# Optimization experiments

Hardware: AMD Instinct MI355X
Metric: run time of the kernel (lower is better)

## Reference

```python
import jax, jax.numpy as jnp
import numpy as np
from jax import lax

B, V, C, H, W = 2, 8, 64, 128, 128
A = 256
C3 = 3 * C + 2  # 194 input channels for refine/confidence branches
CO = 3 * C      # 192 output channels of branch_refine
GROUPS = 8      # _group_count(192, 8) == 8
HID = max(4, CO // 4)  # 48 hidden channels in ChannelGate2d


def _conv3(x, w, b):
    y = lax.conv_general_dilated(x, w, (1, 1), 'SAME',
                                 dimension_numbers=('NCHW', 'OIHW', 'NCHW'))
    return y + b[None, :, None, None]


def _group_norm(x, scale, bias, groups, eps=1e-5):
    b, c, h, w = x.shape
    xg = x.reshape(b, groups, c // groups, h, w)
    mu = xg.mean(axis=(2, 3, 4), keepdims=True)
    var = xg.var(axis=(2, 3, 4), keepdims=True)
    xn = ((xg - mu) / jnp.sqrt(var + eps)).reshape(b, c, h, w)
    return xn * scale[None, :, None, None] + bias[None, :, None, None]


def _channel_gate(x, w1, b1, w2, b2):
    pooled = x.mean(axis=(2, 3))                     # [B,C]
    h = jax.nn.silu(pooled @ w1.T + b1)              # [B,HID]
    gate = jax.nn.sigmoid(h @ w2.T + b2)             # [B,C]
    return x * (0.5 + gate)[:, :, None, None]


def _conv_block(x, p):
    h = jax.nn.silu(_group_norm(_conv3(x, p['c1w'], p['c1b']), p['g1s'], p['g1b'], GROUPS))
    h = jax.nn.silu(_group_norm(_conv3(h, p['c2w'], p['c2b']), p['g2s'], p['g2b'], GROUPS))
    h = _channel_gate(h, p['gw1'], p['gb1'], p['gw2'], p['gb2'])
    res = jnp.einsum('bchw,oc->bohw', x, p['rpw']) + p['rpb'][None, :, None, None]
    return h + jnp.tanh(p['rs']) * res


def _fuse(vf, uvs, masks, importance, atlas_size):
    # vf:[B,V,C,H,W] uvs:[B,V,H,W,2] masks:[B,V,1,H,W] importance:[B,V]
    b, v, c, h, w = vf.shape
    P = atlas_size * atlas_size
    weights = jnp.maximum(importance.astype(vf.dtype), 0.0)
    finite = jnp.isfinite(uvs).all(axis=-1)                 # [B,V,H,W]
    valid = (masks[:, :, 0] > 0.5) & finite & (weights[:, :, None, None] > 0.0)
    safe = jnp.where(finite[..., None], uvs, 0.0)
    xi = jnp.round(jnp.clip(safe[..., 0], 0.0, 1.0) * (atlas_size - 1)).astype(jnp.int32)
    yi = jnp.round((1.0 - jnp.clip(safe[..., 1], 0.0, 1.0)) * (atlas_size - 1)).astype(jnp.int32)
    idx = (yi * atlas_size + xi).reshape(b, v * h * w)      # [B,N]
    wvalid = valid.astype(vf.dtype) * weights[:, :, None, None]
    feat = (vf * wvalid[:, :, None]).transpose(0, 2, 1, 3, 4).reshape(b, c, v * h * w)
    cnt = wvalid.reshape(b, v * h * w)

    def per_sample(f, cc, i):
        atlas = jax.ops.segment_sum(f.T, i, num_segments=P).T   # [C,P]
        counts = jax.ops.segment_sum(cc, i, num_segments=P)     # [P]
        return atlas, counts

    atlas, counts = jax.vmap(per_sample)(feat, cnt, idx)
    atlas = atlas.reshape(b, c, atlas_size, atlas_size)
    counts = counts.reshape(b, 1, atlas_size, atlas_size)
    fused = atlas / jnp.maximum(counts, 1.0)
    return fused, (counts > 0).astype(vf.dtype)


def _normalize_per_sample(t, eps=1e-6):
    scale = jnp.maximum(t.reshape(t.shape[0], -1).max(axis=1), eps)
    return jnp.clip(t / scale[:, None, None, None], 0.0, 1.0)


def setup_inputs() -> dict:
    key = jax.random.key(0)
    ks = jax.random.split(key, 20)
    inp = {
        'encoded_views': jax.random.normal(ks[0], (B, V, C, H, W), jnp.float32),
        'view_uvs': jax.random.uniform(ks[1], (B, V, H, W, 2), jnp.float32),
        'view_masks': jax.random.uniform(ks[2], (B, V, 1, H, W), jnp.float32),
        'w_global': jax.random.uniform(ks[3], (B, V), jnp.float32),
        'w_boundary': jax.random.uniform(ks[4], (B, V), jnp.float32),
        'w_highlight': jax.random.uniform(ks[5], (B, V), jnp.float32),
        'atlas_size': A,
        # ConvBlock params (random instead of zero-init so all paths are exercised)
        'c1w': jax.random.normal(ks[6], (CO, C3, 3, 3), jnp.float32) * 0.02,
        'c1b': jnp.zeros((CO,), jnp.float32),
        'g1s': jnp.ones((CO,), jnp.float32),
        'g1b': jnp.zeros((CO,), jnp.float32),
        'c2w': jax.random.normal(ks[7], (CO, CO, 3, 3), jnp.float32) * 0.02,
        'c2b': jnp.zeros((CO,), jnp.float32),
        'g2s': jnp.ones((CO,), jnp.float32),
        'g2b': jnp.zeros((CO,), jnp.float32),
        'gw1': jax.random.normal(ks[8], (HID, CO), jnp.float32) * 0.05,
        'gb1': jnp.zeros((HID,), jnp.float32),
        'gw2': jax.random.normal(ks[9], (CO, HID), jnp.float32) * 0.05,
        'gb2': jnp.zeros((CO,), jnp.float32),
        'rpw': jax.random.normal(ks[10], (CO, C3), jnp.float32) * 0.05,
        'rpb': jnp.zeros((CO,), jnp.float32),
        'rs': jnp.array(0.3, jnp.float32),
        'conf_w': jax.random.normal(ks[11], (3, C3), jnp.float32) * 0.05,
        'conf_b': jnp.zeros((3,), jnp.float32),
        'mix_scale': jnp.array(0.5, jnp.float32),
    }
    return inp


def reference(encoded_views, view_uvs, view_masks, w_global, w_boundary, w_highlight,
              atlas_size, c1w, c1b, g1s, g1b, c2w, c2b, g2s, g2b,
              gw1, gb1, gw2, gb2, rpw, rpb, rs, conf_w, conf_b, mix_scale):
    p = dict(c1w=c1w, c1b=c1b, g1s=g1s, g1b=g1b, c2w=c2w, c2b=c2b, g2s=g2s, g2b=g2b,
             gw1=gw1, gb1=gb1, gw2=gw2, gb2=gb2, rpw=rpw, rpb=rpb, rs=rs)
    g_feat, g_val = _fuse(encoded_views, view_uvs, view_masks, w_global, atlas_size)
    b_feat, b_val = _fuse(encoded_views, view_uvs, view_masks, w_boundary, atlas_size)
    h_feat, h_val = _fuse(encoded_views, view_uvs, view_masks, w_highlight, atlas_size)
    coverage = jnp.clip((g_val + b_val + h_val) / 3.0, 0.0, 1.0)
    stack = jnp.stack([g_feat, b_feat, h_feat], axis=1)     # [B,3,C,A,A]
    uncertainty = jnp.sqrt(stack.var(axis=1).mean(axis=1, keepdims=True))
    uncertainty = _normalize_per_sample(uncertainty) * coverage
    ctx = jnp.concatenate([g_feat, b_feat, h_feat, coverage, uncertainty], axis=1)
    refine = _conv_block(ctx, p)
    rg, rb, rh = jnp.split(refine, 3, axis=1)
    conf = jax.nn.sigmoid(jnp.einsum('bchw,oc->bohw', ctx, conf_w) + conf_b[None, :, None, None])
    ms = jnp.tanh(mix_scale)
    g_out = g_feat + ms * rg * conf[:, 0:1]
    b_out = b_feat + ms * rb * conf[:, 1:2]
    h_out = h_feat + ms * rh * conf[:, 2:3]
    return (g_out, b_out, h_out, coverage, uncertainty, conf)
```

## Files before the change

kernel.cpp:

```cpp
#include <hip/hip_runtime.h>
#include <math.h>

#define B_ 2
#define V_ 8
#define C_ 64
#define HW_ 16384
#define A_ 256
#define P_ 65536
#define CO_ 192
#define CPG_ 24
#define NG_ 8
#define ICP1 224
#define ICP2 192

#define OFF_ACC   0ull
#define SZ_ACC    (2ull*65536*192*4)
#define OFF_CNT   (OFF_ACC + SZ_ACC)
#define SZ_CNT    (2ull*3*65536*4)
#define OFF_CTXB  (OFF_CNT + SZ_CNT)
#define SZ_CTXB   (2ull*65536*224*2)
#define OFF_H1A   (OFF_CTXB + SZ_CTXB)
#define SZ_H1A    (2ull*65536*192*2)
#define OFF_W1    (OFF_H1A + SZ_H1A)
#define SZ_W1     (9ull*192*224*2)
#define OFF_W2    (OFF_W1 + SZ_W1)
#define SZ_W2     (9ull*192*192*2)
#define OFF_SM    (OFF_W2 + SZ_W2 + 256)

#define SM_STATS1 0
#define SM_STATS2 256
#define SM_SCALE  512
#define SM_POOLED 1024
#define SM_GATE   2560
#define SM_RAWU   8192

#define OUT_B    8388608
#define OUT_COV  25165824
#define OUT_UNC  25296896
#define OUT_CONF 25427968

typedef __attribute__((ext_vector_type(4))) float f32x4;
typedef __attribute__((ext_vector_type(8))) short bf16x8;

__device__ __forceinline__ float sigmoidf_(float x){ return 1.f/(1.f+expf(-x)); }
__device__ __forceinline__ float bf2f(unsigned short h){ return __uint_as_float(((unsigned)h)<<16); }
__device__ __forceinline__ unsigned short f2bf(float f){
  unsigned u = __float_as_uint(f);
  return (unsigned short)((u + 0x7fffu + ((u>>16)&1u)) >> 16);
}

__global__ __launch_bounds__(256) void k_prep(const float* __restrict__ c1w,
    const float* __restrict__ c2w, unsigned short* __restrict__ w1p, unsigned short* __restrict__ w2p)
{
  int idx = blockIdx.x*256 + threadIdx.x;
  const int N1 = 9*192*224;
  if (idx < N1){
    int ic = idx % 224; int oc = (idx/224) % 192; int k = idx/(224*192);
    float v = (ic < 194) ? c1w[(size_t)(oc*194+ic)*9 + k] : 0.f;
    w1p[idx] = f2bf(v);
  } else {
    int i2 = idx - N1;
    if (i2 < 9*192*192){
      int ic = i2 % 192; int oc = (i2/192) % 192; int k = i2/(192*192);
      w2p[i2] = f2bf(c2w[(size_t)(oc*192+ic)*9 + k]);
    }
  }
}

__global__ __launch_bounds__(256) void k_fuse(const float* __restrict__ vf,
    const float* __restrict__ uvs, const float* __restrict__ masks,
    const float* __restrict__ wgp, const float* __restrict__ wbp, const float* __restrict__ whp,
    float* __restrict__ acc, float* __restrict__ cnt)
{
  __shared__ __align__(16) float sf[64*65];
  __shared__ int sidx[64];
  __shared__ int svalid[64];
  __shared__ float sw[3];
  int t = threadIdx.x;
  int pix0 = blockIdx.x*64;
  int b   = pix0 / (V_*HW_);
  int rem = pix0 % (V_*HW_);
  int v   = rem / HW_;
  int p2  = rem % HW_;
  size_t vbase = ((size_t)(b*V_+v))*C_*HW_;
  for (int i=0;i<16;i++){
    int f = t + i*256;
    int c = f>>6, px = f&63;
    sf[c*65+px] = vf[vbase + (size_t)c*HW_ + p2 + px];
  }
  if (t<64){
    const float* u2 = uvs + (((size_t)(b*V_+v))*HW_ + p2 + t)*2;
    float ux = u2[0], uy = u2[1];
    int fin = isfinite(ux) && isfinite(uy);
    float su = fin?ux:0.f, svv = fin?uy:0.f;
    float cu = fminf(fmaxf(su,0.f),1.f);
    float cv = fminf(fmaxf(svv,0.f),1.f);
    int xi = (int)rintf(cu*255.f);
    int yi = (int)rintf((1.f-cv)*255.f);
    sidx[t] = yi*256+xi;
    float m = masks[((size_t)(b*V_+v))*HW_ + p2 + t];
    svalid[t] = (m>0.5f) && fin;
  }
  if (t<3){
    const float* wp = (t==0)?wgp:((t==1)?wbp:whp);
    sw[t] = fmaxf(wp[b*V_+v], 0.f);
  }
  __syncthreads();
  int wave = t>>6, lane = t&63;
  float w0 = sw[0], w1 = sw[1], w2 = sw[2];
  for (int i=0;i<16;i++){
    int px = wave*16+i;
    if (!svalid[px]) continue;
    int bin = sidx[px];
    float val = sf[lane*65+px];
    size_t base = ((size_t)b*P_ + bin)*192;
    if (w0>0.f) atomicAdd(&acc[base + lane],        val*w0);
    if (w1>0.f) atomicAdd(&acc[base + 64 + lane],   val*w1);
    if (w2>0.f) atomicAdd(&acc[base + 128 + lane],  val*w2);
    if (lane<3){
      float wv = sw[lane];
      if (wv>0.f) atomicAdd(&cnt[((size_t)(b*3+lane))*P_ + bin], wv);
    }
  }
}

__global__ __launch_bounds__(256) void k_finalize(const float* __restrict__ acc,
      const float* __restrict__ cnt, unsigned short* __restrict__ ctxb,
      float* __restrict__ out_cov, float* __restrict__ raw_unc, int* __restrict__ scale)
{
  __shared__ __align__(16) float sv[64*193];
  __shared__ float sc[3][64];
  __shared__ float up[256];
  __shared__ float s_cov[64];
  __shared__ float s_unc[64];
  int t = threadIdx.x;
  int bin0 = blockIdx.x*64;
  int b = bin0 >> 16;
  int p0 = bin0 & 65535;
  size_t abase = ((size_t)b*P_ + p0)*192;
  for (int i=0;i<48;i++){
    int f = t + i*256;
    int bl = f/192, c = f - bl*192;
    sv[bl*193+c] = acc[abase + f];
  }
  if (t<192){
    int br = t>>6, bl = t&63;
    sc[br][bl] = cnt[((size_t)(b*3+br))*P_ + p0 + bl];
  }
  __syncthreads();
  {
    int bl = t>>2, q = t&3;
    float dg = 1.f/fmaxf(sc[0][bl],1.f);
    float db = 1.f/fmaxf(sc[1][bl],1.f);
    float dh = 1.f/fmaxf(sc[2][bl],1.f);
    float s = 0.f;
    for (int j=0;j<16;j++){
      int c = q*16+j;
      float fg = sv[bl*193+c]*dg;
      float fb = sv[bl*193+64+c]*db;
      float fh = sv[bl*193+128+c]*dh;
      sv[bl*193+c]=fg; sv[bl*193+64+c]=fb; sv[bl*193+128+c]=fh;
      float m = (fg+fb+fh)*(1.f/3.f);
      float d0=fg-m, d1=fb-m, d2=fh-m;
      s += d0*d0+d1*d1+d2*d2;
    }
    up[t] = s;
  }
  __syncthreads();
  if (t<64){
    float tot = up[t*4]+up[t*4+1]+up[t*4+2]+up[t*4+3];
    float u = sqrtf(tot*(1.f/192.f));
    float vg = sc[0][t]>0.f?1.f:0.f;
    float vb = sc[1][t]>0.f?1.f:0.f;
    float vh = sc[2][t]>0.f?1.f:0.f;
    float cov = fminf(fmaxf((vg+vb+vh)*(1.f/3.f),0.f),1.f);
    s_cov[t] = cov; s_unc[t] = u;
    out_cov[(size_t)b*P_ + p0 + t] = cov;
    raw_unc[(size_t)b*P_ + p0 + t] = u;
    atomicMax(&scale[b], __float_as_int(u));
  }
  __syncthreads();
  for (int f=t; f<1792; f+=256){
    int cg = f % 28, bl = f / 28;
    int c0 = cg*8;
    unsigned short h[8];
    #pragma unroll
    for (int j=0;j<8;j++){
      int c = c0+j;
      float vv;
      if (c < 192)      vv = sv[bl*193+c];
      else if (c==192)  vv = s_cov[bl];
      else if (c==193)  vv = s_unc[bl];
      else              vv = 0.f;
      h[j] = f2bf(vv);
    }
    *(uint4*)&ctxb[((size_t)b*P_ + p0 + bl)*ICP1 + c0] = *(uint4*)h;
  }
}

__global__ __launch_bounds__(256) void k_norm_unc(unsigned short* __restrict__ ctxb,
    const int* __restrict__ scale, const float* __restrict__ raw_unc,
    const float* __restrict__ out_cov, float* __restrict__ out_unc)
{
  int tid = blockIdx.x*256 + threadIdx.x;
  int b = tid >> 16;
  float s = fmaxf(__int_as_float(scale[b]), 1e-6f);
  float u = raw_unc[tid];
  float cov = out_cov[tid];
  float un = fminf(fmaxf(u/s,0.f),1.f)*cov;
  out_unc[tid] = un;
  ctxb[(size_t)tid*ICP1 + 193] = f2bf(un);
}

template<int ICP, int CHUNKS>
__global__ __launch_bounds__(256,4) void k_conv3(const unsigned short* __restrict__ X,
    const unsigned short* __restrict__ Wp, const float* __restrict__ bias, float* __restrict__ Y)
{
  __shared__ short s_in[258*32];
  __shared__ short s_w[192*32];
  int t = threadIdx.x;
  int y0 = blockIdx.x;
  int oc0 = blockIdx.y*64;
  int b = blockIdx.z;
  int wv = t>>6, lane = t&63, l15 = lane&15, quad = lane>>4;
  f32x4 acc[4][4];
  #pragma unroll
  for (int mt=0;mt<4;mt++){
    float4 bv = *(const float4*)&bias[oc0 + mt*16 + quad*4];
    f32x4 iv; iv.x=bv.x; iv.y=bv.y; iv.z=bv.z; iv.w=bv.w;
    #pragma unroll
    for (int nt=0;nt<4;nt++) acc[mt][nt]=iv;
  }
  const unsigned short* Xb = X + (size_t)b*P_*ICP;
  for (int ch=0; ch<CHUNKS; ++ch){
    int ic0 = ch*32;
    for (int ky=0; ky<3; ky++){
      int gy = y0 + ky - 1;
      if ((unsigned)gy >= 256u) continue;
      __syncthreads();
      for (int f=t; f<1032; f+=256){
        int icq = f&3, xi = f>>2;
        int gx = xi - 1;
        uint4 vval = make_uint4(0,0,0,0);
        if ((unsigned)gx < 256u)
          vval = *(const uint4*)&Xb[(size_t)(gy*256+gx)*ICP + ic0 + icq*8];
        *(uint4*)&s_in[xi*32 + ((icq ^ ((xi>>1)&3)))*8] = vval;
      }
      for (int f=t; f<768; f+=256){
        int icq = f&3, oc = (f>>2)&63, kx = f>>8;
        uint4 vval = *(const uint4*)&Wp[(size_t)((ky*3+kx)*192 + oc0 + oc)*ICP + ic0 + icq*8];
        int r = kx*64 + oc;
        *(uint4*)&s_w[r*32 + ((icq ^ ((r>>1)&3)))*8] = vval;
      }
      __syncthreads();
      #pragma unroll
      for (int kx=0;kx<3;kx++){
        bf16x8 Af[4], Bf[4];
        #pragma unroll
        for (int mt=0;mt<4;mt++){
          int r = kx*64 + mt*16 + l15;
          Af[mt] = *(const bf16x8*)&s_w[r*32 + (((quad ^ ((r>>1)&3)))&3)*8];
        }
        #pragma unroll
        for (int nt=0;nt<4;nt++){
          int r = wv*64 + nt*16 + l15 + kx;
          Bf[nt] = *(const bf16x8*)&s_in[r*32 + (((quad ^ ((r>>1)&3)))&3)*8];
        }
        #pragma unroll
        for (int mt=0;mt<4;mt++)
          #pragma unroll
          for (int nt=0;nt<4;nt++)
            acc[mt][nt] = __builtin_amdgcn_mfma_f32_16x16x32_bf16(Af[mt], Bf[nt], acc[mt][nt], 0, 0, 0);
      }
    }
  }
  float* Yb = Y + (size_t)b*P_*192;
  #pragma unroll
  for (int mt=0;mt<4;mt++){
    int oc = oc0 + mt*16 + quad*4;
    #pragma unroll
    for (int nt=0;nt<4;nt++){
      int px = wv*64 + nt*16 + l15;
      *(f32x4*)&Yb[(size_t)(y0*256+px)*192 + oc] = acc[mt][nt];
    }
  }
}

__global__ __launch_bounds__(256) void k_gn_stats(const float* __restrict__ x, double* __restrict__ stats)
{
  int b = blockIdx.y; int y0 = blockIdx.x*2;
  const float* base = x + ((size_t)b*P_ + y0*256)*192;
  int t = threadIdx.x;
  double s1[3]={0,0,0}, s2[3]={0,0,0};
  for (int j=0;j<96;j++){
    int f4 = t + j*256;
    float4 v = *(const float4*)&base[(size_t)f4*4];
    int r = j - (j/3)*3;
    s1[r] += (double)v.x + (double)v.y + (double)v.z + (double)v.w;
    s2[r] += (double)v.x*v.x + (double)v.y*v.y + (double)v.z*v.z + (double)v.w*v.w;
  }
  __shared__ double red[16];
  if (t<16) red[t]=0.0;
  __syncthreads();
  #pragma unroll
  for (int r=0;r<3;r++){
    int c = (4*t + 64*r) % 192;
    int g = c/24;
    atomicAdd(&red[g*2],   s1[r]);
    atomicAdd(&red[g*2+1], s2[r]);
  }
  __syncthreads();
  if (t<8){
    atomicAdd(&stats[(b*8+t)*2],   red[t*2]);
    atomicAdd(&stats[(b*8+t)*2+1], red[t*2+1]);
  }
}

__global__ __launch_bounds__(256) void k_gn1_apply(const float* __restrict__ x, const double* __restrict__ stats,
    const float* __restrict__ gs, const float* __restrict__ gb, unsigned short* __restrict__ y)
{
  size_t i8 = ((size_t)blockIdx.x*256 + threadIdx.x)*8;
  int b = (int)(i8 / ((size_t)192*P_));
  int c = (int)(i8 % 192);
  int bg = b*8 + c/24;
  const double N = 24.0*65536.0;
  double mu = stats[bg*2]/N;
  double var = stats[bg*2+1]/N - mu*mu;
  float rstd = 1.0f/sqrtf((float)var + 1e-5f);
  float mean = (float)mu;
  float4 sA = *(const float4*)&gs[c];
  float4 sB = *(const float4*)&gs[c+4];
  float4 bA = *(const float4*)&gb[c];
  float4 bB = *(const float4*)&gb[c+4];
  float4 v0 = *(const float4*)&x[i8];
  float4 v1 = *(const float4*)&x[i8+4];
  float xin[8] = {v0.x,v0.y,v0.z,v0.w,v1.x,v1.y,v1.z,v1.w};
  float scl[8] = {sA.x,sA.y,sA.z,sA.w,sB.x,sB.y,sB.z,sB.w};
  float bia[8] = {bA.x,bA.y,bA.z,bA.w,bB.x,bB.y,bB.z,bB.w};
  unsigned short h[8];
  #pragma unroll
  for (int i=0;i<8;i++){
    float xn = (xin[i]-mean)*rstd*scl[i] + bia[i];
    h[i] = f2bf(xn*sigmoidf_(xn));
  }
  *(uint4*)&y[i8] = *(uint4*)h;
}

__global__ __launch_bounds__(256) void k_gn2_apply(float* __restrict__ x, const double* __restrict__ stats,
    const float* __restrict__ gs, const float* __restrict__ gb)
{
  size_t i8 = ((size_t)blockIdx.x*256 + threadIdx.x)*8;
  int b = (int)(i8 / ((size_t)192*P_));
  int c = (int)(i8 % 192);
  int bg = b*8 + c/24;
  const double N = 24.0*65536.0;
  double mu = stats[bg*2]/N;
  double var = stats[bg*2+1]/N - mu*mu;
  float rstd = 1.0f/sqrtf((float)var + 1e-5f);
  float mean = (float)mu;
  float4 sA = *(const float4*)&gs[c];
  float4 sB = *(const float4*)&gs[c+4];
  float4 bA = *(const float4*)&gb[c];
  float4 bB = *(const float4*)&gb[c+4];
  float4 v0 = *(const float4*)&x[i8];
  float4 v1 = *(const float4*)&x[i8+4];
  float xin[8] = {v0.x,v0.y,v0.z,v0.w,v1.x,v1.y,v1.z,v1.w};
  float scl[8] = {sA.x,sA.y,sA.z,sA.w,sB.x,sB.y,sB.z,sB.w};
  float bia[8] = {bA.x,bA.y,bA.z,bA.w,bB.x,bB.y,bB.z,bB.w};
  #pragma unroll
  for (int i=0;i<8;i++){
    float xn = (xin[i]-mean)*rstd*scl[i] + bia[i];
    xin[i] = xn*sigmoidf_(xn);
  }
  *(float4*)&x[i8]   = make_float4(xin[0],xin[1],xin[2],xin[3]);
  *(float4*)&x[i8+4] = make_float4(xin[4],xin[5],xin[6],xin[7]);
}

__global__ __launch_bounds__(256) void k_pool(const float* __restrict__ x, float* __restrict__ pooled)
{
  int b = blockIdx.y; int y0 = blockIdx.x*4;
  const float* base = x + ((size_t)b*P_ + y0*256)*192;
  int t = threadIdx.x;
  float4 p[3];
  #pragma unroll
  for (int r=0;r<3;r++) p[r] = make_float4(0.f,0.f,0.f,0.f);
  for (int j=0;j<192;j++){
    int f4 = t + j*256;
    float4 v = *(const float4*)&base[(size_t)f4*4];
    int r = j - (j/3)*3;
    p[r].x += v.x; p[r].y += v.y; p[r].z += v.z; p[r].w += v.w;
  }
  __shared__ float pl[192];
  if (t<192) pl[t]=0.f;
  __syncthreads();
  #pragma unroll
  for (int r=0;r<3;r++){
    int c = (4*t + 64*r) % 192;
    atomicAdd(&pl[c],   p[r].x);
    atomicAdd(&pl[c+1], p[r].y);
    atomicAdd(&pl[c+2], p[r].z);
    atomicAdd(&pl[c+3], p[r].w);
  }
  __syncthreads();
  if (t<192) atomicAdd(&pooled[b*192+t], pl[t]*(1.f/65536.f));
}

__global__ void k_gate(const float* __restrict__ pooled, const float* __restrict__ gw1,
    const float* __restrict__ gb1, const float* __restrict__ gw2, const float* __restrict__ gb2,
    float* __restrict__ gatef)
{
  __shared__ float hb[2*48];
  int t = threadIdx.x;
  if (t<96){
    int b=t/48, j=t%48;
    float a = gb1[j];
    for (int c=0;c<192;c++) a = fmaf(pooled[b*192+c], gw1[j*192+c], a);
    hb[t] = a*sigmoidf_(a);
  }
  __syncthreads();
  for (int i=t;i<384;i+=256){
    int b=i/192, c=i%192;
    float a = gb2[c];
    for (int j=0;j<48;j++) a = fmaf(hb[b*48+j], gw2[c*48+j], a);
    gatef[i] = 0.5f + sigmoidf_(a);
  }
}

__global__ __launch_bounds__(256) void k_conf(const unsigned short* __restrict__ ctxb,
    const float* __restrict__ cw, const float* __restrict__ cbias, float* __restrict__ out_conf)
{
  __shared__ float scw[3*224];
  int t = threadIdx.x;
  for (int f=t; f<672; f+=256){
    int c = f % 224, o = f / 224;
    scw[f] = (c<194) ? cw[o*194 + c] : 0.f;
  }
  __syncthreads();
  int tid = blockIdx.x*256 + t;
  int b = tid >> 16, p = tid & 65535;
  const unsigned short* cp = ctxb + ((size_t)b*P_ + p)*ICP1;
  float a0 = cbias[0], a1 = cbias[1], a2 = cbias[2];
  for (int q=0;q<28;q++){
    uint4 v = *(const uint4*)&cp[q*8];
    unsigned wd[4] = {v.x,v.y,v.z,v.w};
    #pragma unroll
    for (int j=0;j<8;j++){
      unsigned bits = wd[j>>1];
      float xf = (j&1) ? __uint_as_float(bits & 0xffff0000u) : __uint_as_float(bits<<16);
      int c = q*8+j;
      a0 = fmaf(xf, scw[c],       a0);
      a1 = fmaf(xf, scw[224+c],   a1);
      a2 = fmaf(xf, scw[448+c],   a2);
    }
  }
  out_conf[((size_t)(b*3+0))*P_ + p] = sigmoidf_(a0);
  out_conf[((size_t)(b*3+1))*P_ + p] = sigmoidf_(a1);
  out_conf[((size_t)(b*3+2))*P_ + p] = sigmoidf_(a2);
}

__global__ __launch_bounds__(256,4) void k_combine(const unsigned short* __restrict__ ctxb,
    const float* __restrict__ h2, const float* __restrict__ rpw, const float* __restrict__ rpb,
    const float* __restrict__ gatef, const float* __restrict__ conf_out,
    const float* __restrict__ rs, const float* __restrict__ mix, float* __restrict__ dout)
{
  __shared__ short s_x[256*32];
  __shared__ short s_w[64*32];
  int t = threadIdx.x;
  size_t p0 = (size_t)blockIdx.x*256;
  int oc0 = blockIdx.y*64, br = blockIdx.y;
  int wv = t>>6, lane = t&63, l15 = lane&15, quad = lane>>4;
  f32x4 acc[4][4];
  #pragma unroll
  for (int mt=0;mt<4;mt++){
    float4 bv = *(const float4*)&rpb[oc0 + mt*16 + quad*4];
    f32x4 iv; iv.x=bv.x; iv.y=bv.y; iv.z=bv.z; iv.w=bv.w;
    #pragma unroll
    for (int nt=0;nt<4;nt++) acc[mt][nt]=iv;
  }
  for (int ch=0; ch<7; ch++){
    int ic0 = ch*32;
    __syncthreads();
    for (int f=t; f<1024; f+=256){
      int icq = f&3, px = f>>2;
      uint4 v = *(const uint4*)&ctxb[(p0+px)*ICP1 + ic0 + icq*8];
      *(uint4*)&s_x[px*32 + ((icq ^ ((px>>1)&3)))*8] = v;
    }
    {
      int oc = t&63, icq = t>>6;
      unsigned short h[8];
      #pragma unroll
      for (int j=0;j<8;j++){
        int ic = ic0 + icq*8 + j;
        h[j] = (ic<194) ? f2bf(rpw[(size_t)(oc0+oc)*194 + ic]) : (unsigned short)0;
      }
      *(uint4*)&s_w[oc*32 + ((icq ^ ((oc>>1)&3)))*8] = *(uint4*)h;
    }
    __syncthreads();
    bf16x8 Af[4], Bf[4];
    #pragma unroll
    for (int mt=0;mt<4;mt++){
      int r = mt*16 + l15;
      Af[mt] = *(const bf16x8*)&s_w[r*32 + (((quad ^ ((r>>1)&3)))&3)*8];
    }
    #pragma unroll
    for (int nt=0;nt<4;nt++){
      int r = wv*64 + nt*16 + l15;
      Bf[nt] = *(const bf16x8*)&s_x[r*32 + (((quad ^ ((r>>1)&3)))&3)*8];
    }
    #pragma unroll
    for (int mt=0;mt<4;mt++)
      #pragma unroll
      for (int nt=0;nt<4;nt++)
        acc[mt][nt] = __builtin_amdgcn_mfma_f32_16x16x32_bf16(Af[mt], Bf[nt], acc[mt][nt], 0, 0, 0);
  }
  float trs = tanhf(rs[0]);
  float ms2 = tanhf(mix[0]);
  int b = (int)(p0 >> 16);
  #pragma unroll
  for (int mt=0;mt<4;mt++){
    int oc = oc0 + mt*16 + quad*4;
    int cc = oc & 63;
    float4 gv = *(const float4*)&gatef[b*192 + oc];
    #pragma unroll
    for (int nt=0;nt<4;nt++){
      size_t pf = p0 + wv*64 + nt*16 + l15;
      int p = (int)(pf & 65535);
      ushort4 fh = *(const ushort4*)&ctxb[pf*ICP1 + oc];
      float4 hv = *(const float4*)&h2[pf*192 + oc];
      float cf = conf_out[((size_t)(b*3+br))*P_ + p];
      size_t dst = (size_t)br*OUT_B + ((size_t)(b*64+cc))*P_ + p;
      dout[dst]            = bf2f(fh.x) + ms2*(hv.x*gv.x + trs*acc[mt][nt].x)*cf;
      dout[dst + P_]       = bf2f(fh.y) + ms2*(hv.y*gv.y + trs*acc[mt][nt].y)*cf;
      dout[dst + 2*P_]     = bf2f(fh.z) + ms2*(hv.z*gv.z + trs*acc[mt][nt].z)*cf;
      dout[dst + 3*P_]     = bf2f(fh.w) + ms2*(hv.w*gv.w + trs*acc[mt][nt].w)*cf;
    }
  }
}

extern "C" void kernel_launch(void* const* d_in, const int* in_sizes, int n_in,
                              void* d_out, int out_size, void* d_ws, size_t ws_size,
                              hipStream_t stream)
{
  const float* vf    = (const float*)d_in[0];
  const float* uvs   = (const float*)d_in[1];
  const float* masks = (const float*)d_in[2];
  const float* wg    = (const float*)d_in[3];
  const float* wb    = (const float*)d_in[4];
  const float* wh    = (const float*)d_in[5];
  const float* c1w = (const float*)d_in[7];
  const float* c1b = (const float*)d_in[8];
  const float* g1s = (const float*)d_in[9];
  const float* g1b = (const float*)d_in[10];
  const float* c2w = (const float*)d_in[11];
  const float* c2b = (const float*)d_in[12];
  const float* g2s = (const float*)d_in[13];
  const float* g2b = (const float*)d_in[14];
  const float* gw1 = (const float*)d_in[15];
  const float* gb1 = (const float*)d_in[16];
  const float* gw2 = (const float*)d_in[17];
  const float* gb2 = (const float*)d_in[18];
  const float* rpw = (const float*)d_in[19];
  const float* rpb = (const float*)d_in[20];
  const float* rs  = (const float*)d_in[21];
  const float* cw  = (const float*)d_in[22];
  const float* cb  = (const float*)d_in[23];
  const float* mix = (const float*)d_in[24];

  char* ws = (char*)d_ws;
  float*          accb  = (float*)(ws + OFF_ACC);
  float*          cntb  = (float*)(ws + OFF_CNT);
  unsigned short* ctxb  = (unsigned short*)(ws + OFF_CTXB);
  unsigned short* h1act = (unsigned short*)(ws + OFF_H1A);
  unsigned short* w1p   = (unsigned short*)(ws + OFF_W1);
  unsigned short* w2p   = (unsigned short*)(ws + OFF_W2);
  float*  h1raw  = (float*)(ws + OFF_ACC);
  float*  h2     = (float*)(ws + OFF_ACC);
  double* stats1 = (double*)(ws + OFF_SM + SM_STATS1);
  double* stats2 = (double*)(ws + OFF_SM + SM_STATS2);
  int*    scale  = (int*)(ws + OFF_SM + SM_SCALE);
  float*  pooled = (float*)(ws + OFF_SM + SM_POOLED);
  float*  gatef  = (float*)(ws + OFF_SM + SM_GATE);
  float*  rawu   = (float*)(ws + OFF_SM + SM_RAWU);

  float* out = (float*)d_out;
  float* out_cov  = out + OUT_COV;
  float* out_unc  = out + OUT_UNC;
  float* out_conf = out + OUT_CONF;

  hipMemsetAsync(ws + OFF_ACC, 0, SZ_ACC + SZ_CNT, stream);
  hipMemsetAsync(ws + OFF_SM, 0, 8192, stream);

  k_prep<<<2808, 256, 0, stream>>>(c1w, c2w, w1p, w2p);
  k_fuse<<<4096, 256, 0, stream>>>(vf, uvs, masks, wg, wb, wh, accb, cntb);
  k_finalize<<<2048, 256, 0, stream>>>(accb, cntb, ctxb, out_cov, rawu, scale);
  k_norm_unc<<<512, 256, 0, stream>>>(ctxb, scale, rawu, out_cov, out_unc);
  k_conv3<ICP1,7><<<dim3(256,3,2), 256, 0, stream>>>(ctxb, w1p, c1b, h1raw);
  k_gn_stats<<<dim3(128,2), 256, 0, stream>>>(h1raw, stats1);
  k_gn1_apply<<<12288, 256, 0, stream>>>(h1raw, stats1, g1s, g1b, h1act);
  k_conv3<ICP2,6><<<dim3(256,3,2), 256, 0, stream>>>(h1act, w2p, c2b, h2);
  k_gn_stats<<<dim3(128,2), 256, 0, stream>>>(h2, stats2);
  k_gn2_apply<<<12288, 256, 0, stream>>>(h2, stats2, g2s, g2b);
  k_pool<<<dim3(64,2), 256, 0, stream>>>(h2, pooled);
  k_gate<<<1, 256, 0, stream>>>(pooled, gw1, gb1, gw2, gb2, gatef);
  k_conf<<<512, 256, 0, stream>>>(ctxb, cw, cb, out_conf);
  k_combine<<<dim3(512,3), 256, 0, stream>>>(ctxb, h2, rpw, rpb, gatef, out_conf, rs, mix, out);
}
```

Before: 863.4 us.

## Fuse GroupNorm stats into conv epilogue, pool into GN2, conf into combine; two rows per conv block

Each conv3 block now computes two output rows. It loads four input rows once per channel chunk and reloads only the weights per ky, so input staging is reused across rows. GroupNorm sum and sum-of-squares are reduced in the conv epilogue with shuffles and shared/global atomics, which removes the separate stats pass over the fp32 output. Global average pooling moves into the GN2 apply kernel via shared atomics, and the confidence dot product moves into k_combine using the staged input tile. Risks: lower occupancy from the larger LDS and register footprint, float rather than double per-block stat accumulation, and heavy shared atomics in gn2_apply.

```diff
diff --git a/kernel.cpp b/kernel.cpp
--- a/kernel.cpp
+++ b/kernel.cpp
@@ -8,8 +8,6 @@
 #define A_ 256
 #define P_ 65536
 #define CO_ 192
-#define CPG_ 24
-#define NG_ 8
 #define ICP1 224
 #define ICP2 192
 
@@ -213,106 +211,129 @@
 }
 
 template<int ICP, int CHUNKS>
-__global__ __launch_bounds__(256,4) void k_conv3(const unsigned short* __restrict__ X,
-    const unsigned short* __restrict__ Wp, const float* __restrict__ bias, float* __restrict__ Y)
-{
-  __shared__ short s_in[258*32];
+__global__ __launch_bounds__(256,2) void k_conv3(const unsigned short* __restrict__ X,
+    const unsigned short* __restrict__ Wp, const float* __restrict__ bias, float* __restrict__ Y,
+    double* __restrict__ stats)
+{
+  __shared__ short s_in[4*258*32];
   __shared__ short s_w[192*32];
+  __shared__ float sgn[16];
   int t = threadIdx.x;
-  int y0 = blockIdx.x;
+  int y0 = blockIdx.x*2;
   int oc0 = blockIdx.y*64;
   int b = blockIdx.z;
   int wv = t>>6, lane = t&63, l15 = lane&15, quad = lane>>4;
-  f32x4 acc[4][4];
+  if (t<16) sgn[t]=0.f;
+  f32x4 acc[2][4][4];
   #pragma unroll
   for (int mt=0;mt<4;mt++){
     float4 bv = *(const float4*)&bias[oc0 + mt*16 + quad*4];
     f32x4 iv; iv.x=bv.x; iv.y=bv.y; iv.z=bv.z; iv.w=bv.w;
     #pragma unroll
-    for (int nt=0;nt<4;nt++) acc[mt][nt]=iv;
+    for (int rr=0;rr<2;rr++)
+      #pragma unroll
+      for (int nt=0;nt<4;nt++) acc[rr][mt][nt]=iv;
   }
   const unsigned short* Xb = X + (size_t)b*P_*ICP;
   for (int ch=0; ch<CHUNKS; ++ch){
     int ic0 = ch*32;
+    __syncthreads();
+    for (int f=t; f<4128; f+=256){
+      int row = f/1032; int rem = f - row*1032;
+      int xi = rem>>2, icq = rem&3;
+      int gx = xi - 1, gy = y0 - 1 + row;
+      uint4 vval = make_uint4(0,0,0,0);
+      if ((unsigned)gx < 256u && (unsigned)gy < 256u)
+        vval = *(const uint4*)&Xb[(size_t)(gy*256+gx)*ICP + ic0 + icq*8];
+      *(uint4*)&s_in[row*8256 + xi*32 + ((icq ^ ((xi>>1)&3)))*8] = vval;
+    }
+    for (int f=t; f<768; f+=256){
+      int icq = f&3, oc = (f>>2)&63, kx = f>>8;
+      uint4 vval = *(const uint4*)&Wp[(size_t)((0*3+kx)*192 + oc0 + oc)*ICP + ic0 + icq*8];
+      int r = kx*64 + oc;
+      *(uint4*)&s_w[r*32 + ((icq ^ ((r>>1)&3)))*8] = vval;
+    }
+    __syncthreads();
     for (int ky=0; ky<3; ky++){
-      int gy = y0 + ky - 1;
-      if ((unsigned)gy >= 256u) continue;
-      __syncthreads();
-      for (int f=t; f<1032; f+=256){
-        int icq = f&3, xi = f>>2;
-        int gx = xi - 1;
-        uint4 vval = make_uint4(0,0,0,0);
-        if ((unsigned)gx < 256u)
-          vval = *(const uint4*)&Xb[(size_t)(gy*256+gx)*ICP + ic0 + icq*8];
-        *(uint4*)&s_in[xi*32 + ((icq ^ ((xi>>1)&3)))*8] = vval;
-      }
-      for (int f=t; f<768; f+=256){
-        int icq = f&3, oc = (f>>2)&63, kx = f>>8;
-        uint4 vval = *(const uint4*)&Wp[(size_t)((ky*3+kx)*192 + oc0 + oc)*ICP + ic0 + icq*8];
-        int r = kx*64 + oc;
-        *(uint4*)&s_w[r*32 + ((icq ^ ((r>>1)&3)))*8] = vval;
-      }
-      __syncthreads();
       #pragma unroll
       for (int kx=0;kx<3;kx++){
-        bf16x8 Af[4], Bf[4];
+        bf16x8 Af[4], Bf[2][4];
         #pragma unroll
         for (int mt=0;mt<4;mt++){
           int r = kx*64 + mt*16 + l15;
           Af[mt] = *(const bf16x8*)&s_w[r*32 + (((quad ^ ((r>>1)&3)))&3)*8];
         }
         #pragma unroll
-        for (int nt=0;nt<4;nt++){
-          int r = wv*64 + nt*16 + l15 + kx;
-          Bf[nt] = *(const bf16x8*)&s_in[r*32 + (((quad ^ ((r>>1)&3)))&3)*8];
+        for (int rr=0;rr<2;rr++){
+          int ri = rr + ky;
+          #pragma unroll
+          for (int nt=0;nt<4;nt++){
+            int x = wv*64 + nt*16 + l15 + kx;
+            Bf[rr][nt] = *(const bf16x8*)&s_in[ri*8256 + x*32 + (((quad ^ ((x>>1)&3)))&3)*8];
+          }
         }
         #pragma unroll
         for (int mt=0;mt<4;mt++)
           #pragma unroll
-          for (int nt=0;nt<4;nt++)
-            acc[mt][nt] = __builtin_amdgcn_mfma_f32_16x16x32_bf16(Af[mt], Bf[nt], acc[mt][nt], 0, 0, 0);
+          for (int rr=0;rr<2;rr++)
+            #pragma unroll
+            for (int nt=0;nt<4;nt++)
+              acc[rr][mt][nt] = __builtin_amdgcn_mfma_f32_16x16x32_bf16(Af[mt], Bf[rr][nt], acc[rr][mt][nt], 0, 0, 0);
+      }
+      if (ky<2){
+        __syncthreads();
+        for (int f=t; f<768; f+=256){
+          int icq = f&3, oc = (f>>2)&63, kx = f>>8;
+          uint4 vval = *(const uint4*)&Wp[(size_t)(((ky+1)*3+kx)*192 + oc0 + oc)*ICP + ic0 + icq*8];
+          int r = kx*64 + oc;
+          *(uint4*)&s_w[r*32 + ((icq ^ ((r>>1)&3)))*8] = vval;
+        }
+        __syncthreads();
       }
     }
   }
   float* Yb = Y + (size_t)b*P_*192;
   #pragma unroll
+  for (int rr=0;rr<2;rr++){
+    int y = y0 + rr;
+    #pragma unroll
+    for (int mt=0;mt<4;mt++){
+      int oc = oc0 + mt*16 + quad*4;
+      #pragma unroll
+      for (int nt=0;nt<4;nt++){
+        int px = wv*64 + nt*16 + l15;
+        *(f32x4*)&Yb[(size_t)(y*256+px)*192 + oc] = acc[rr][mt][nt];
+      }
+    }
+  }
+  #pragma unroll
   for (int mt=0;mt<4;mt++){
-    int oc = oc0 + mt*16 + quad*4;
-    #pragma unroll
-    for (int nt=0;nt<4;nt++){
-      int px = wv*64 + nt*16 + l15;
-      *(f32x4*)&Yb[(size_t)(y0*256+px)*192 + oc] = acc[mt][nt];
-    }
-  }
-}
-
-__global__ __launch_bounds__(256) void k_gn_stats(const float* __restrict__ x, double* __restrict__ stats)
-{
-  int b = blockIdx.y; int y0 = blockIdx.x*2;
-  const float* base = x + ((size_t)b*P_ + y0*256)*192;
-  int t = threadIdx.x;
-  double s1[3]={0,0,0}, s2[3]={0,0,0};
-  for (int j=0;j<96;j++){
-    int f4 = t + j*256;
-    float4 v = *(const float4*)&base[(size_t)f4*4];
-    int r = j - (j/3)*3;
-    s1[r] += (double)v.x + (double)v.y + (double)v.z + (double)v.w;
-    s2[r] += (double)v.x*v.x + (double)v.y*v.y + (double)v.z*v.z + (double)v.w*v.w;
-  }
-  __shared__ double red[16];
-  if (t<16) red[t]=0.0;
-  __syncthreads();
-  #pragma unroll
-  for (int r=0;r<3;r++){
-    int c = (4*t + 64*r) % 192;
-    int g = c/24;
-    atomicAdd(&red[g*2],   s1[r]);
-    atomicAdd(&red[g*2+1], s2[r]);
-  }
-  __syncthreads();
-  if (t<8){
-    atomicAdd(&stats[(b*8+t)*2],   red[t*2]);
-    atomicAdd(&stats[(b*8+t)*2+1], red[t*2+1]);
+    #pragma unroll
+    for (int j=0;j<4;j++){
+      float s=0.f, q=0.f;
+      #pragma unroll
+      for (int rr=0;rr<2;rr++)
+        #pragma unroll
+        for (int nt=0;nt<4;nt++){
+          float vv = acc[rr][mt][nt][j];
+          s += vv; q += vv*vv;
+        }
+      #pragma unroll
+      for (int off=1; off<16; off<<=1){
+        s += __shfl_xor(s, off);
+        q += __shfl_xor(q, off);
+      }
+      if (l15==0){
+        int g = (oc0 + mt*16 + quad*4 + j)/24;
+        atomicAdd(&sgn[(g&7)*2],   s);
+        atomicAdd(&sgn[(g&7)*2+1], q);
+      }
+    }
+  }
+  __syncthreads();
+  if (t<16){
+    int g = t>>1;
+    atomicAdd(&stats[(size_t)(b*8+g)*2 + (t&1)], (double)sgn[t]);
   }
 }
 
@@ -347,9 +368,13 @@
 }
 
 __global__ __launch_bounds__(256) void k_gn2_apply(float* __restrict__ x, const double* __restrict__ stats,
-    const float* __restrict__ gs, const float* __restrict__ gb)
-{
-  size_t i8 = ((size_t)blockIdx.x*256 + threadIdx.x)*8;
+    const float* __restrict__ gs, const float* __restrict__ gb, float* __restrict__ pooled)
+{
+  __shared__ float pl[192];
+  int t = threadIdx.x;
+  if (t<192) pl[t]=0.f;
+  __syncthreads();
+  size_t i8 = ((size_t)blockIdx.x*256 + t)*8;
   int b = (int)(i8 / ((size_t)192*P_));
   int c = (int)(i8 % 192);
   int bg = b*8 + c/24;
@@ -374,35 +399,10 @@
   }
   *(float4*)&x[i8]   = make_float4(xin[0],xin[1],xin[2],xin[3]);
   *(float4*)&x[i8+4] = make_float4(xin[4],xin[5],xin[6],xin[7]);
-}
-
-__global__ __launch_bounds__(256) void k_pool(const float* __restrict__ x, float* __restrict__ pooled)
-{
-  int b = blockIdx.y; int y0 = blockIdx.x*4;
-  const float* base = x + ((size_t)b*P_ + y0*256)*192;
-  int t = threadIdx.x;
-  float4 p[3];
-  #pragma unroll
-  for (int r=0;r<3;r++) p[r] = make_float4(0.f,0.f,0.f,0.f);
-  for (int j=0;j<192;j++){
-    int f4 = t + j*256;
-    float4 v = *(const float4*)&base[(size_t)f4*4];
-    int r = j - (j/3)*3;
-    p[r].x += v.x; p[r].y += v.y; p[r].z += v.z; p[r].w += v.w;
-  }
-  __shared__ float pl[192];
-  if (t<192) pl[t]=0.f;
-  __syncthreads();
-  #pragma unroll
-  for (int r=0;r<3;r++){
-    int c = (4*t + 64*r) % 192;
-    atomicAdd(&pl[c],   p[r].x);
-    atomicAdd(&pl[c+1], p[r].y);
-    atomicAdd(&pl[c+2], p[r].z);
-    atomicAdd(&pl[c+3], p[r].w);
-  }
-  __syncthreads();
-  if (t<192) atomicAdd(&pooled[b*192+t], pl[t]*(1.f/65536.f));
+  #pragma unroll
+  for (int i=0;i<8;i++) atomicAdd(&pl[c+i], xin[i]);
+  __syncthreads();
+  if (t<192) atomicAdd(&pooled[b*192+t], pl[t]);
 }
 
 __global__ void k_gate(const float* __restrict__ pooled, const float* __restrict__ gw1,
@@ -411,10 +411,11 @@
 {
   __shared__ float hb[2*48];
   int t = threadIdx.x;
+  const float inv = 1.f/65536.f;
   if (t<96){
     int b=t/48, j=t%48;
     float a = gb1[j];
-    for (int c=0;c<192;c++) a = fmaf(pooled[b*192+c], gw1[j*192+c], a);
+    for (int c=0;c<192;c++) a = fmaf(pooled[b*192+c]*inv, gw1[j*192+c], a);
     hb[t] = a*sigmoidf_(a);
   }
   __syncthreads();
@@ -426,49 +427,22 @@
   }
 }
 
-__global__ __launch_bounds__(256) void k_conf(const unsigned short* __restrict__ ctxb,
-    const float* __restrict__ cw, const float* __restrict__ cbias, float* __restrict__ out_conf)
-{
-  __shared__ float scw[3*224];
-  int t = threadIdx.x;
-  for (int f=t; f<672; f+=256){
-    int c = f % 224, o = f / 224;
-    scw[f] = (c<194) ? cw[o*194 + c] : 0.f;
-  }
-  __syncthreads();
-  int tid = blockIdx.x*256 + t;
-  int b = tid >> 16, p = tid & 65535;
-  const unsigned short* cp = ctxb + ((size_t)b*P_ + p)*ICP1;
-  float a0 = cbias[0], a1 = cbias[1], a2 = cbias[2];
-  for (int q=0;q<28;q++){
-    uint4 v = *(const uint4*)&cp[q*8];
-    unsigned wd[4] = {v.x,v.y,v.z,v.w};
-    #pragma unroll
-    for (int j=0;j<8;j++){
-      unsigned bits = wd[j>>1];
-      float xf = (j&1) ? __uint_as_float(bits & 0xffff0000u) : __uint_as_float(bits<<16);
-      int c = q*8+j;
-      a0 = fmaf(xf, scw[c],       a0);
-      a1 = fmaf(xf, scw[224+c],   a1);
-      a2 = fmaf(xf, scw[448+c],   a2);
-    }
-  }
-  out_conf[((size_t)(b*3+0))*P_ + p] = sigmoidf_(a0);
-  out_conf[((size_t)(b*3+1))*P_ + p] = sigmoidf_(a1);
-  out_conf[((size_t)(b*3+2))*P_ + p] = sigmoidf_(a2);
-}
-
 __global__ __launch_bounds__(256,4) void k_combine(const unsigned short* __restrict__ ctxb,
     const float* __restrict__ h2, const float* __restrict__ rpw, const float* __restrict__ rpb,
-    const float* __restrict__ gatef, const float* __restrict__ conf_out,
-    const float* __restrict__ rs, const float* __restrict__ mix, float* __restrict__ dout)
+    const float* __restrict__ gatef, const float* __restrict__ cw, const float* __restrict__ cbias,
+    const float* __restrict__ rs, const float* __restrict__ mix,
+    float* __restrict__ out_conf, float* __restrict__ dout)
 {
   __shared__ short s_x[256*32];
   __shared__ short s_w[64*32];
+  __shared__ float s_cw[224];
+  __shared__ float s_conf[256];
   int t = threadIdx.x;
   size_t p0 = (size_t)blockIdx.x*256;
   int oc0 = blockIdx.y*64, br = blockIdx.y;
   int wv = t>>6, lane = t&63, l15 = lane&15, quad = lane>>4;
+  if (t<224) s_cw[t] = (t<194) ? cw[br*194+t] : 0.f;
+  float cdot = cbias[br];
   f32x4 acc[4][4];
   #pragma unroll
   for (int mt=0;mt<4;mt++){
@@ -477,6 +451,7 @@
     #pragma unroll
     for (int nt=0;nt<4;nt++) acc[mt][nt]=iv;
   }
+  int myxor = (t>>1)&3;
   for (int ch=0; ch<7; ch++){
     int ic0 = ch*32;
     __syncthreads();
@@ -496,6 +471,17 @@
       *(uint4*)&s_w[oc*32 + ((icq ^ ((oc>>1)&3)))*8] = *(uint4*)h;
     }
     __syncthreads();
+    #pragma unroll
+    for (int icq=0; icq<4; icq++){
+      uint4 v = *(const uint4*)&s_x[t*32 + ((icq ^ myxor))*8];
+      unsigned wd[4] = {v.x,v.y,v.z,v.w};
+      #pragma unroll
+      for (int j=0;j<8;j++){
+        unsigned bits = wd[j>>1];
+        float xf = (j&1) ? __uint_as_float(bits & 0xffff0000u) : __uint_as_float(bits<<16);
+        cdot = fmaf(xf, s_cw[ic0 + icq*8 + j], cdot);
+      }
+    }
     bf16x8 Af[4], Bf[4];
     #pragma unroll
     for (int mt=0;mt<4;mt++){
@@ -513,9 +499,15 @@
       for (int nt=0;nt<4;nt++)
         acc[mt][nt] = __builtin_amdgcn_mfma_f32_16x16x32_bf16(Af[mt], Bf[nt], acc[mt][nt], 0, 0, 0);
   }
+  int b = (int)(p0 >> 16);
+  {
+    float cfv = sigmoidf_(cdot);
+    s_conf[t] = cfv;
+    out_conf[(size_t)(b*3+br)*P_ + ((p0 + t) & 65535)] = cfv;
+  }
+  __syncthreads();
   float trs = tanhf(rs[0]);
   float ms2 = tanhf(mix[0]);
-  int b = (int)(p0 >> 16);
   #pragma unroll
   for (int mt=0;mt<4;mt++){
     int oc = oc0 + mt*16 + quad*4;
@@ -523,16 +515,17 @@
     float4 gv = *(const float4*)&gatef[b*192 + oc];
     #pragma unroll
     for (int nt=0;nt<4;nt++){
-      size_t pf = p0 + wv*64 + nt*16 + l15;
+      int pl = wv*64 + nt*16 + l15;
+      size_t pf = p0 + pl;
       int p = (int)(pf & 65535);
       ushort4 fh = *(const ushort4*)&ctxb[pf*ICP1 + oc];
       float4 hv = *(const float4*)&h2[pf*192 + oc];
-      float cf = conf_out[((size_t)(b*3+br))*P_ + p];
+      float cf = s_conf[pl];
       size_t dst = (size_t)br*OUT_B + ((size_t)(b*64+cc))*P_ + p;
-      dout[dst]            = bf2f(fh.x) + ms2*(hv.x*gv.x + trs*acc[mt][nt].x)*cf;
-      dout[dst + P_]       = bf2f(fh.y) + ms2*(hv.y*gv.y + trs*acc[mt][nt].y)*cf;
-      dout[dst + 2*P_]     = bf2f(fh.z) + ms2*(hv.z*gv.z + trs*acc[mt][nt].z)*cf;
-      dout[dst + 3*P_]     = bf2f(fh.w) + ms2*(hv.w*gv.w + trs*acc[mt][nt].w)*cf;
+      dout[dst]        = bf2f(fh.x) + ms2*(hv.x*gv.x + trs*acc[mt][nt].x)*cf;
+      dout[dst + P_]   = bf2f(fh.y) + ms2*(hv.y*gv.y + trs*acc[mt][nt].y)*cf;
+      dout[dst + 2*P_] = bf2f(fh.z) + ms2*(hv.z*gv.z + trs*acc[mt][nt].z)*cf;
+      dout[dst + 3*P_] = bf2f(fh.w) + ms2*(hv.w*gv.w + trs*acc[mt][nt].w)*cf;
     }
   }
 }
@@ -594,14 +587,10 @@
   k_fuse<<<4096, 256, 0, stream>>>(vf, uvs, masks, wg, wb, wh, accb, cntb);
   k_finalize<<<2048, 256, 0, stream>>>(accb, cntb, ctxb, out_cov, rawu, scale);
   k_norm_unc<<<512, 256, 0, stream>>>(ctxb, scale, rawu, out_cov, out_unc);
-  k_conv3<ICP1,7><<<dim3(256,3,2), 256, 0, stream>>>(ctxb, w1p, c1b, h1raw);
-  k_gn_stats<<<dim3(128,2), 256, 0, stream>>>(h1raw, stats1);
+  k_conv3<ICP1,7><<<dim3(128,3,2), 256, 0, stream>>>(ctxb, w1p, c1b, h1raw, stats1);
   k_gn1_apply<<<12288, 256, 0, stream>>>(h1raw, stats1, g1s, g1b, h1act);
-  k_conv3<ICP2,6><<<dim3(256,3,2), 256, 0, stream>>>(h1act, w2p, c2b, h2);
-  k_gn_stats<<<dim3(128,2), 256, 0, stream>>>(h2, stats2);
-  k_gn2_apply<<<12288, 256, 0, stream>>>(h2, stats2, g2s, g2b);
-  k_pool<<<dim3(64,2), 256, 0, stream>>>(h2, pooled);
+  k_conv3<ICP2,6><<<dim3(128,3,2), 256, 0, stream>>>(h1act, w2p, c2b, h2, stats2);
+  k_gn2_apply<<<12288, 256, 0, stream>>>(h2, stats2, g2s, g2b, pooled);
   k_gate<<<1, 256, 0, stream>>>(pooled, gw1, gb1, gw2, gb2, gatef);
-  k_conf<<<512, 256, 0, stream>>>(ctxb, cw, cb, out_conf);
-  k_combine<<<dim3(512,3), 256, 0, stream>>>(ctxb, h2, rpw, rpb, gatef, out_conf, rs, mix, out);
-}
+  k_combine<<<dim3(512,3), 256, 0, stream>>>(ctxb, h2, rpw, rpb, gatef, cw, cb, rs, mix, out_conf, out);
+}
```

Measured after the change: 1.100 ms. 1.27x slower.
